# Optimization experiments

Hardware: AMD Instinct MI355X
Metric: run time of the kernel (lower is better)

The kernel has to match this reference:

```python
import jax, jax.numpy as jnp
import numpy as np

HIDDEN = 256
HEADS = 8
DK = HIDDEN // HEADS
BH = 16  # bias_h_size
N = 2048
B = 1


def setup_inputs() -> dict:
    key = jax.random.key(0)
    ks = jax.random.split(key, 20)
    s = 0.02
    inp = {
        "int_chain_label": jax.random.randint(ks[0], (N, N), 0, 2, dtype=jnp.int32),
        "dist_map": jax.random.uniform(ks[1], (N, N), dtype=jnp.float32),
        "contact_map": jax.random.uniform(ks[2], (N, N), dtype=jnp.float32),
        "q": jax.random.normal(ks[3], (B, N, HIDDEN), dtype=jnp.float32),
        "k": jax.random.normal(ks[4], (B, N, HIDDEN), dtype=jnp.float32),
        "v": jax.random.normal(ks[5], (B, N, HIDDEN), dtype=jnp.float32),
        # projections
        "Wq": jax.random.normal(ks[6], (HIDDEN, HIDDEN), dtype=jnp.float32) * s,
        "bq": jnp.zeros((HIDDEN,), jnp.float32),
        "Wk": jax.random.normal(ks[7], (HIDDEN, HIDDEN), dtype=jnp.float32) * s,
        "bk": jnp.zeros((HIDDEN,), jnp.float32),
        "Wv": jax.random.normal(ks[8], (HIDDEN, HIDDEN), dtype=jnp.float32) * s,
        "bv": jnp.zeros((HIDDEN,), jnp.float32),
        "Wo": jax.random.normal(ks[9], (HIDDEN, HIDDEN), dtype=jnp.float32) * s,
        "bo": jnp.zeros((HIDDEN,), jnp.float32),
        # distance bias MLP: Linear(2, BH) -> Linear(BH, 1)
        "Wd1": jax.random.normal(ks[10], (2, BH), dtype=jnp.float32) * 0.5,
        "bd1": jnp.zeros((BH,), jnp.float32),
        "Wd2": jax.random.normal(ks[11], (BH, 1), dtype=jnp.float32) * 0.5,
        "bd2": jnp.zeros((1,), jnp.float32),
        # contact bias MLP
        "Wc1": jax.random.normal(ks[12], (2, BH), dtype=jnp.float32) * 0.5,
        "bc1": jnp.zeros((BH,), jnp.float32),
        "Wc2": jax.random.normal(ks[13], (BH, 1), dtype=jnp.float32) * 0.5,
        "bc2": jnp.zeros((1,), jnp.float32),
    }
    return inp


def _pair_bias(mp, label_f, W1, b1, W2, b2):
    # stack(map, label) -> [N,N,2]; two linears (no nonlinearity in original) -> [N,N]
    x = jnp.stack((mp, label_f), axis=-1)
    h = x @ W1 + b1                      # [N,N,BH]
    return (h @ W2 + b2)[..., 0]          # [N,N]


def reference(int_chain_label, dist_map, contact_map, q, k, v,
              Wq, bq, Wk, bk, Wv, bv, Wo, bo,
              Wd1, bd1, Wd2, bd2, Wc1, bc1, Wc2, bc2):
    label_f = int_chain_label.astype(jnp.float32)
    bias = (_pair_bias(dist_map, label_f, Wd1, bd1, Wd2, bd2)
            + _pair_bias(contact_map, label_f, Wc1, bc1, Wc2, bc2))  # [N,N]
    bias = bias[None, None]  # [1,1,N,N] broadcast over batch, heads

    b, n, _ = q.shape
    scale = DK ** -0.5
    qh = (q @ Wq + bq).reshape(b, n, HEADS, DK).transpose(0, 2, 1, 3) * scale  # [B,H,N,D]
    kh = (k @ Wk + bk).reshape(b, n, HEADS, DK).transpose(0, 2, 1, 3)
    vh = (v @ Wv + bv).reshape(b, n, HEADS, DK).transpose(0, 2, 1, 3)

    scores = jnp.einsum('bhnd,bhmd->bhnm', qh, kh) + bias  # [B,H,N,N]
    attn = jax.nn.softmax(scores, axis=-1)
    out = jnp.einsum('bhnm,bhmd->bhnd', attn, vh)           # [B,H,N,D]
    out = out.transpose(0, 2, 1, 3).reshape(b, n, HEADS * DK)
    return out @ Wo + bo
```

## Files before the change

### kernel.cpp

```cpp
#include <hip/hip_runtime.h>
#include <hip/hip_bf16.h>

#define SN 2048
#define HD 256
#define NHEAD 8
#define DK 32
#define BH 16

typedef __bf16 bf16;
typedef __bf16 bf16x8 __attribute__((ext_vector_type(8)));
typedef __bf16 bf16x4 __attribute__((ext_vector_type(4)));
typedef float f32x4 __attribute__((ext_vector_type(4)));
typedef int i32x4 __attribute__((ext_vector_type(4)));
typedef unsigned uint4v __attribute__((ext_vector_type(4)));

__global__ void __launch_bounds__(256) prep_wt_kernel(
    const float* __restrict__ Wq, const float* __restrict__ Wk,
    const float* __restrict__ Wv, const float* __restrict__ Wo,
    bf16* __restrict__ wt)
{
    __shared__ bf16 tile[32][HD + 8];
    int mat = blockIdx.x >> 3, rc = blockIdx.x & 7;
    int t = threadIdx.x;
    const float* W = mat == 0 ? Wq : mat == 1 ? Wk : mat == 2 ? Wv : Wo;
    bf16* Wt = wt + mat * HD * HD;
    int r0 = rc * 32;
    #pragma unroll
    for (int i = 0; i < 32; i++) tile[i][t] = (bf16)W[(r0 + i) * HD + t];
    __syncthreads();
    #pragma unroll
    for (int i = 0; i < 32; i++) Wt[t * HD + r0 + i] = tile[i][t];
}

template<bool AF32, int MODE, bool OUTF32>
__device__ __forceinline__ void gemm_body(
    const void* __restrict__ Ap, const bf16* __restrict__ Wt,
    const float* __restrict__ bias, void* __restrict__ outp, int bid)
{
    int wave = threadIdx.x >> 6, lane = threadIdx.x & 63;
    int g = lane >> 4, qi = lane & 15;
    int mblk = bid & 31, nblk = bid >> 5;
    int m0 = mblk * 64 + wave * 16, n0 = nblk * 32;
    f32x4 acc0 = {0.f, 0.f, 0.f, 0.f}, acc1 = {0.f, 0.f, 0.f, 0.f};
    const bf16* W0 = Wt + (n0 + qi) * HD + 8 * g;
    const bf16* W1 = W0 + 16 * HD;

    auto loadA = [&](int ks) -> bf16x8 {
        if constexpr (AF32) {
            const float* Ar = (const float*)Ap + (m0 + qi) * HD + 8 * g + ks * 32;
            f32x4 lo = *(const f32x4*)Ar;
            f32x4 hi = *(const f32x4*)(Ar + 4);
            bf16x8 a;
            #pragma unroll
            for (int e = 0; e < 4; e++) { a[e] = (bf16)lo[e]; a[4 + e] = (bf16)hi[e]; }
            return a;
        } else {
            return *(const bf16x8*)((const bf16*)Ap + (m0 + qi) * HD + 8 * g + ks * 32);
        }
    };

    bf16x8 a_c  = loadA(0);
    bf16x8 b0_c = *(const bf16x8*)(W0);
    bf16x8 b1_c = *(const bf16x8*)(W1);
    #pragma unroll
    for (int ks = 0; ks < 8; ks++) {
        bf16x8 a_n, b0_n, b1_n;
        if (ks < 7) {
            a_n  = loadA(ks + 1);
            b0_n = *(const bf16x8*)(W0 + (ks + 1) * 32);
            b1_n = *(const bf16x8*)(W1 + (ks + 1) * 32);
        }
        acc0 = __builtin_amdgcn_mfma_f32_16x16x32_bf16(a_c, b0_c, acc0, 0, 0, 0);
        acc1 = __builtin_amdgcn_mfma_f32_16x16x32_bf16(a_c, b1_c, acc1, 0, 0, 0);
        if (ks < 7) { a_c = a_n; b0_c = b0_n; b1_c = b1_n; }
    }
    float bv0 = bias[n0 + qi], bv1 = bias[n0 + 16 + qi];
    if constexpr (MODE == 0) {
        if constexpr (OUTF32) {
            float* out = (float*)outp;
            #pragma unroll
            for (int r = 0; r < 4; r++) {
                int m = m0 + 4 * g + r;
                out[m * HD + n0 + qi]      = acc0[r] + bv0;
                out[m * HD + n0 + 16 + qi] = acc1[r] + bv1;
            }
        } else {
            bf16* out = (bf16*)outp;
            #pragma unroll
            for (int r = 0; r < 4; r++) {
                int m = m0 + 4 * g + r;
                out[m * HD + n0 + qi]      = (bf16)(acc0[r] + bv0);
                out[m * HD + n0 + 16 + qi] = (bf16)(acc1[r] + bv1);
            }
        }
    } else {
        bf16* out = (bf16*)outp;
        bf16x4 v0, v1;
        #pragma unroll
        for (int r = 0; r < 4; r++) { v0[r] = (bf16)(acc0[r] + bv0); v1[r] = (bf16)(acc1[r] + bv1); }
        *(bf16x4*)(out + (n0 + qi) * SN + m0 + 4 * g)      = v0;
        *(bf16x4*)(out + (n0 + 16 + qi) * SN + m0 + 4 * g) = v1;
    }
}

__global__ void __launch_bounds__(256) qkv_kernel(
    const float* __restrict__ q, const float* __restrict__ k, const float* __restrict__ v,
    const bf16* __restrict__ wt,
    const float* __restrict__ bq, const float* __restrict__ bk, const float* __restrict__ bv,
    bf16* __restrict__ qh, bf16* __restrict__ kh, bf16* __restrict__ vt)
{
    int w = blockIdx.y;
    if (w == 0)      gemm_body<true, 0, false>(q, wt,               bq, qh, blockIdx.x);
    else if (w == 1) gemm_body<true, 0, false>(k, wt + HD * HD,     bk, kh, blockIdx.x);
    else             gemm_body<true, 1, false>(v, wt + 2 * HD * HD, bv, vt, blockIdx.x);
}

__global__ void __launch_bounds__(256) oproj_kernel(
    const bf16* __restrict__ A, const bf16* __restrict__ wt3,
    const float* __restrict__ bo, float* __restrict__ out)
{
    gemm_body<false, 0, true>(A, wt3, bo, out, blockIdx.x);
}

template<int KCHT>
__global__ void __launch_bounds__(128) attn_kernel(
    const bf16* __restrict__ qh, const bf16* __restrict__ kh,
    const bf16* __restrict__ vt,
    const int* __restrict__ label, const float* __restrict__ dist,
    const float* __restrict__ contact,
    const float* __restrict__ Wd1, const float* __restrict__ bd1,
    const float* __restrict__ Wd2, const float* __restrict__ bd2,
    const float* __restrict__ Wc1, const float* __restrict__ bc1,
    const float* __restrict__ Wc2, const float* __restrict__ bc2,
    float* __restrict__ po, float* __restrict__ pm, float* __restrict__ pl)
{
    constexpr int KT = SN / KCHT / 64;
    int wave = threadIdx.x >> 6, lane = threadIdx.x & 63;
    int g = lane >> 4, qi = lane & 15;
    int h = blockIdx.x / (64 * KCHT);
    int rem = blockIdx.x % (64 * KCHT);
    int qb = rem / KCHT, c = rem % KCHT;
    int q0 = qb * 32 + wave * 16;
    int kbase = c * (KT * 64);

    float ad = 0.f, bld = 0.f, dd = bd2[0];
    #pragma unroll
    for (int j = 0; j < BH; j++) {
        float w2 = Wd2[j];
        ad  += Wd1[j] * w2;
        bld += Wd1[BH + j] * w2;
        dd  += bd1[j] * w2;
    }
    float ac = 0.f, blc = 0.f, dc = bc2[0];
    #pragma unroll
    for (int j = 0; j < BH; j++) {
        float w2 = Wc2[j];
        ac  += Wc1[j] * w2;
        blc += Wc1[BH + j] * w2;
        dc  += bc1[j] * w2;
    }
    float bl = bld + blc, dl = dd + dc;

    bf16x8 qf = *(const bf16x8*)(qh + (q0 + qi) * HD + h * DK + 8 * g);
    const bf16* kp  = kh + h * DK + 8 * g + kbase * HD;
    const bf16* v0p = vt + (h * DK + qi) * SN + 8 * g + kbase;
    const bf16* v1p = v0p + 16 * SN;
    const float* dp = dist    + (q0 + qi) * SN + 4 * g + kbase;
    const float* cp = contact + (q0 + qi) * SN + 4 * g + kbase;
    const int*   lp = label   + (q0 + qi) * SN + 4 * g + kbase;

    const float scale = 0.17677669529663687f;
    float m = -1e30f, lsum = 0.f;
    f32x4 o0 = {0.f, 0.f, 0.f, 0.f}, o1 = {0.f, 0.f, 0.f, 0.f};

    int src0 = ((lane >> 4) & 1) * 32 + (lane & 15);
    int src1 = src0 + 16;
    bool hi = lane >= 32;

    #pragma unroll
    for (int kt = 0; kt < KT; kt++) {
        int key0 = kt * 64;
        bf16x8 kf0 = *(const bf16x8*)(kp + (key0 +  0 + qi) * HD);
        bf16x8 kf1 = *(const bf16x8*)(kp + (key0 + 16 + qi) * HD);
        bf16x8 kf2 = *(const bf16x8*)(kp + (key0 + 32 + qi) * HD);
        bf16x8 kf3 = *(const bf16x8*)(kp + (key0 + 48 + qi) * HD);
        f32x4 dv0 = *(const f32x4*)(dp + key0 +  0), dv1 = *(const f32x4*)(dp + key0 + 16);
        f32x4 dv2 = *(const f32x4*)(dp + key0 + 32), dv3 = *(const f32x4*)(dp + key0 + 48);
        f32x4 cv0 = *(const f32x4*)(cp + key0 +  0), cv1 = *(const f32x4*)(cp + key0 + 16);
        f32x4 cv2 = *(const f32x4*)(cp + key0 + 32), cv3 = *(const f32x4*)(cp + key0 + 48);
        i32x4 lv0 = *(const i32x4*)(lp + key0 +  0), lv1 = *(const i32x4*)(lp + key0 + 16);
        i32x4 lv2 = *(const i32x4*)(lp + key0 + 32), lv3 = *(const i32x4*)(lp + key0 + 48);
        bf16x8 va00 = *(const bf16x8*)(v0p + key0);
        bf16x8 va01 = *(const bf16x8*)(v0p + key0 + 32);
        bf16x8 va10 = *(const bf16x8*)(v1p + key0);
        bf16x8 va11 = *(const bf16x8*)(v1p + key0 + 32);

        f32x4 zero = {0.f, 0.f, 0.f, 0.f};
        f32x4 s0 = __builtin_amdgcn_mfma_f32_16x16x32_bf16(kf0, qf, zero, 0, 0, 0);
        f32x4 s1 = __builtin_amdgcn_mfma_f32_16x16x32_bf16(kf1, qf, zero, 0, 0, 0);
        f32x4 s2 = __builtin_amdgcn_mfma_f32_16x16x32_bf16(kf2, qf, zero, 0, 0, 0);
        f32x4 s3 = __builtin_amdgcn_mfma_f32_16x16x32_bf16(kf3, qf, zero, 0, 0, 0);
        float x[16];
        #pragma unroll
        for (int r = 0; r < 4; r++) {
            float b0 = ad * dv0[r] + ac * cv0[r] + bl * (float)lv0[r] + dl;
            float b1 = ad * dv1[r] + ac * cv1[r] + bl * (float)lv1[r] + dl;
            float b2 = ad * dv2[r] + ac * cv2[r] + bl * (float)lv2[r] + dl;
            float b3 = ad * dv3[r] + ac * cv3[r] + bl * (float)lv3[r] + dl;
            x[r]      = s0[r] * scale + b0;
            x[4 + r]  = s1[r] * scale + b1;
            x[8 + r]  = s2[r] * scale + b2;
            x[12 + r] = s3[r] * scale + b3;
        }
        float t0 = fmaxf(x[0], x[1]),   t1 = fmaxf(x[2], x[3]);
        float t2 = fmaxf(x[4], x[5]),   t3 = fmaxf(x[6], x[7]);
        float t4 = fmaxf(x[8], x[9]),   t5 = fmaxf(x[10], x[11]);
        float t6 = fmaxf(x[12], x[13]), t7 = fmaxf(x[14], x[15]);
        float tm = fmaxf(fmaxf(fmaxf(t0, t1), fmaxf(t2, t3)),
                         fmaxf(fmaxf(t4, t5), fmaxf(t6, t7)));
        tm = fmaxf(tm, __shfl_xor(tm, 16));
        tm = fmaxf(tm, __shfl_xor(tm, 32));
        float mnew = fmaxf(m, tm);
        float f = __expf(m - mnew);
        float ps = 0.f;
        #pragma unroll
        for (int i = 0; i < 16; i++) { x[i] = __expf(x[i] - mnew); ps += x[i]; }
        ps += __shfl_xor(ps, 16);
        ps += __shfl_xor(ps, 32);
        lsum = lsum * f + ps;
        m = mnew;
        #pragma unroll
        for (int r = 0; r < 4; r++) { o0[r] *= f; o1[r] *= f; }

        auto PK = [](float a, float b) -> int {
            unsigned short ua = __builtin_bit_cast(unsigned short, (bf16)a);
            unsigned short ub = __builtin_bit_cast(unsigned short, (bf16)b);
            return (int)((unsigned)ua | ((unsigned)ub << 16));
        };
        int c0 = PK(x[0], x[1]),  c1 = PK(x[2], x[3]);
        int c2 = PK(x[4], x[5]),  c3 = PK(x[6], x[7]);
        int c4 = PK(x[8], x[9]),  c5 = PK(x[10], x[11]);
        int c6 = PK(x[12], x[13]), c7 = PK(x[14], x[15]);

        unsigned a00 = (unsigned)__shfl(c0, src0), a01 = (unsigned)__shfl(c2, src0);
        unsigned a10 = (unsigned)__shfl(c1, src0), a11 = (unsigned)__shfl(c3, src0);
        unsigned a20 = (unsigned)__shfl(c0, src1), a21 = (unsigned)__shfl(c2, src1);
        unsigned a30 = (unsigned)__shfl(c1, src1), a31 = (unsigned)__shfl(c3, src1);
        unsigned b00 = (unsigned)__shfl(c4, src0), b01 = (unsigned)__shfl(c6, src0);
        unsigned b10 = (unsigned)__shfl(c5, src0), b11 = (unsigned)__shfl(c7, src0);
        unsigned b20 = (unsigned)__shfl(c4, src1), b21 = (unsigned)__shfl(c6, src1);
        unsigned b30 = (unsigned)__shfl(c5, src1), b31 = (unsigned)__shfl(c7, src1);
        uint4v u0 = { hi ? a01 : a00, hi ? a11 : a10, hi ? a21 : a20, hi ? a31 : a30 };
        uint4v u1 = { hi ? b01 : b00, hi ? b11 : b10, hi ? b21 : b20, hi ? b31 : b30 };
        bf16x8 pb0 = __builtin_bit_cast(bf16x8, u0);
        bf16x8 pb1 = __builtin_bit_cast(bf16x8, u1);

        o0 = __builtin_amdgcn_mfma_f32_16x16x32_bf16(va00, pb0, o0, 0, 0, 0);
        o0 = __builtin_amdgcn_mfma_f32_16x16x32_bf16(va01, pb1, o0, 0, 0, 0);
        o1 = __builtin_amdgcn_mfma_f32_16x16x32_bf16(va10, pb0, o1, 0, 0, 0);
        o1 = __builtin_amdgcn_mfma_f32_16x16x32_bf16(va11, pb1, o1, 0, 0, 0);
    }
    int hq = h * SN + q0 + qi;
    *(f32x4*)(po + (hq * KCHT + c) * DK + 4 * g)      = o0;
    *(f32x4*)(po + (hq * KCHT + c) * DK + 16 + 4 * g) = o1;
    if (g == 0) { pm[hq * KCHT + c] = m; pl[hq * KCHT + c] = lsum; }
}

template<int KCHT>
__global__ void __launch_bounds__(256) combine_kernel(
    const float* __restrict__ po, const float* __restrict__ pm,
    const float* __restrict__ pl, bf16* __restrict__ aout)
{
    int idx = blockIdx.x * 256 + threadIdx.x;
    int d = idx & (DK - 1), hq = idx >> 5;
    int h = hq >> 11, qr = hq & (SN - 1);
    float mv[KCHT], lv[KCHT];
    #pragma unroll
    for (int c = 0; c < KCHT; c++) { mv[c] = pm[hq * KCHT + c]; lv[c] = pl[hq * KCHT + c]; }
    float M = mv[0];
    #pragma unroll
    for (int c = 1; c < KCHT; c++) M = fmaxf(M, mv[c]);
    float L = 0.f, o = 0.f;
    const float* p = po + hq * KCHT * DK + d;
    #pragma unroll
    for (int c = 0; c < KCHT; c++) {
        float w = __expf(mv[c] - M);
        L += w * lv[c];
        o += w * p[c * DK];
    }
    aout[qr * HD + h * DK + d] = (bf16)(o / L);
}

extern "C" void kernel_launch(void* const* d_in, const int* in_sizes, int n_in,
                              void* d_out, int out_size, void* d_ws, size_t ws_size,
                              hipStream_t stream)
{
    static const int expect[22] = {
        SN * SN, SN * SN, SN * SN,
        SN * HD, SN * HD, SN * HD,
        HD * HD, HD, HD * HD, HD,
        HD * HD, HD, HD * HD, HD,
        2 * BH, BH, BH, 1,
        2 * BH, BH, BH, 1
    };
    if (n_in != 22) return;
    for (int i = 0; i < 22; i++) if (in_sizes[i] != expect[i]) return;

    const int*   label   = (const int*)  d_in[0];
    const float* dist    = (const float*)d_in[1];
    const float* contact = (const float*)d_in[2];
    const float* q  = (const float*)d_in[3];
    const float* k  = (const float*)d_in[4];
    const float* v  = (const float*)d_in[5];
    const float* Wq = (const float*)d_in[6];  const float* bq = (const float*)d_in[7];
    const float* Wk = (const float*)d_in[8];  const float* bk = (const float*)d_in[9];
    const float* Wv = (const float*)d_in[10]; const float* bv = (const float*)d_in[11];
    const float* Wo = (const float*)d_in[12]; const float* bo = (const float*)d_in[13];
    const float* Wd1 = (const float*)d_in[14]; const float* bd1 = (const float*)d_in[15];
    const float* Wd2 = (const float*)d_in[16]; const float* bd2 = (const float*)d_in[17];
    const float* Wc1 = (const float*)d_in[18]; const float* bc1 = (const float*)d_in[19];
    const float* Wc2 = (const float*)d_in[20]; const float* bc2 = (const float*)d_in[21];

    char* ws = (char*)d_ws;
    bf16*  qh   = (bf16*)(ws);
    bf16*  kh   = (bf16*)(ws + (1u << 20));
    bf16*  vt   = (bf16*)(ws + (2u << 20));
    bf16*  aout = (bf16*)(ws + (3u << 20));
    bf16*  wt   = (bf16*)(ws + (4u << 20));
    float* po   = (float*)(ws + (5u << 20));

    prep_wt_kernel<<<dim3(32), 256, 0, stream>>>(Wq, Wk, Wv, Wo, wt);
    qkv_kernel<<<dim3(256, 3), 256, 0, stream>>>(q, k, v, wt, bq, bk, bv, qh, kh, vt);

    size_t need8 = (5u << 20) + (size_t)NHEAD * SN * 8 * DK * 4 + 2u * NHEAD * SN * 8 * 4;
    if (ws_size >= need8 + (1u << 20)) {
        float* pm = (float*)(ws + (5u << 20) + (size_t)NHEAD * SN * 8 * DK * 4);
        float* pl = pm + NHEAD * SN * 8;
        attn_kernel<8><<<dim3(NHEAD * 64 * 8), 128, 0, stream>>>(
            qh, kh, vt, label, dist, contact,
            Wd1, bd1, Wd2, bd2, Wc1, bc1, Wc2, bc2, po, pm, pl);
        combine_kernel<8><<<dim3(NHEAD * SN * DK / 256), 256, 0, stream>>>(po, pm, pl, aout);
    } else {
        float* pm = (float*)(ws + (13u << 20));
        float* pl = pm + NHEAD * SN * 4;
        attn_kernel<4><<<dim3(NHEAD * 64 * 4), 128, 0, stream>>>(
            qh, kh, vt, label, dist, contact,
            Wd1, bd1, Wd2, bd2, Wc1, bc1, Wc2, bc2, po, pm, pl);
        combine_kernel<4><<<dim3(NHEAD * SN * DK / 256), 256, 0, stream>>>(po, pm, pl, aout);
    }

    oproj_kernel<<<dim3(256), 256, 0, stream>>>(aout, wt + 3 * HD * HD, bo, (float*)d_out);
}
```

Baseline: 222.7 us.

## Precompute head-shared pair bias plane once instead of per-head

Adds a prep stage that collapses the dist, contact and label maps into a single fp32 bias plane, written to the workspace before attention. The attention kernel then reads one float stream per key instead of three and skips the per-element bias arithmetic, which was previously repeated for each of the 8 heads. This costs an extra read of three N×N maps and a write of one N×N plane up front, and needs more workspace. A fallback path keeps the old inline computation for small workspaces.

```diff
diff --git a/kernel.cpp b/kernel.cpp
--- a/kernel.cpp
+++ b/kernel.cpp
@@ -14,22 +14,62 @@
 typedef int i32x4 __attribute__((ext_vector_type(4)));
 typedef unsigned uint4v __attribute__((ext_vector_type(4)));
 
-__global__ void __launch_bounds__(256) prep_wt_kernel(
+__global__ void __launch_bounds__(256) prep_kernel(
     const float* __restrict__ Wq, const float* __restrict__ Wk,
     const float* __restrict__ Wv, const float* __restrict__ Wo,
-    bf16* __restrict__ wt)
-{
-    __shared__ bf16 tile[32][HD + 8];
-    int mat = blockIdx.x >> 3, rc = blockIdx.x & 7;
+    const int* __restrict__ label, const float* __restrict__ dist,
+    const float* __restrict__ contact,
+    const float* __restrict__ Wd1, const float* __restrict__ bd1,
+    const float* __restrict__ Wd2, const float* __restrict__ bd2,
+    const float* __restrict__ Wc1, const float* __restrict__ bc1,
+    const float* __restrict__ Wc2, const float* __restrict__ bc2,
+    bf16* __restrict__ wt, float* __restrict__ plane)
+{
+    int bid = blockIdx.x;
     int t = threadIdx.x;
-    const float* W = mat == 0 ? Wq : mat == 1 ? Wk : mat == 2 ? Wv : Wo;
-    bf16* Wt = wt + mat * HD * HD;
-    int r0 = rc * 32;
-    #pragma unroll
-    for (int i = 0; i < 32; i++) tile[i][t] = (bf16)W[(r0 + i) * HD + t];
-    __syncthreads();
-    #pragma unroll
-    for (int i = 0; i < 32; i++) Wt[t * HD + r0 + i] = tile[i][t];
+    if (bid < 32) {
+        __shared__ bf16 tile[32][HD + 8];
+        int mat = bid >> 3, rc = bid & 7;
+        const float* W = mat == 0 ? Wq : mat == 1 ? Wk : mat == 2 ? Wv : Wo;
+        bf16* Wt = wt + mat * HD * HD;
+        int r0 = rc * 32;
+        #pragma unroll
+        for (int i = 0; i < 32; i++) tile[i][t] = (bf16)W[(r0 + i) * HD + t];
+        __syncthreads();
+        #pragma unroll
+        for (int i = 0; i < 32; i++) Wt[t * HD + r0 + i] = tile[i][t];
+        return;
+    }
+    float ad = 0.f, bld = 0.f, dd = bd2[0];
+    #pragma unroll
+    for (int j = 0; j < BH; j++) {
+        float w2 = Wd2[j];
+        ad  += Wd1[j] * w2;
+        bld += Wd1[BH + j] * w2;
+        dd  += bd1[j] * w2;
+    }
+    float ac = 0.f, blc = 0.f, dc = bc2[0];
+    #pragma unroll
+    for (int j = 0; j < BH; j++) {
+        float w2 = Wc2[j];
+        ac  += Wc1[j] * w2;
+        blc += Wc1[BH + j] * w2;
+        dc  += bc1[j] * w2;
+    }
+    float bl = bld + blc, dl = dd + dc;
+
+    int base = (bid - 32) * 2048 + t * 8;
+    f32x4 d0 = *(const f32x4*)(dist + base),    d1 = *(const f32x4*)(dist + base + 4);
+    f32x4 c0 = *(const f32x4*)(contact + base), c1 = *(const f32x4*)(contact + base + 4);
+    i32x4 l0 = *(const i32x4*)(label + base),   l1 = *(const i32x4*)(label + base + 4);
+    f32x4 o0, o1;
+    #pragma unroll
+    for (int e = 0; e < 4; e++) {
+        o0[e] = ad * d0[e] + ac * c0[e] + bl * (float)l0[e] + dl;
+        o1[e] = ad * d1[e] + ac * c1[e] + bl * (float)l1[e] + dl;
+    }
+    *(f32x4*)(plane + base)     = o0;
+    *(f32x4*)(plane + base + 4) = o1;
 }
 
 template<bool AF32, int MODE, bool OUTF32>
@@ -122,10 +162,10 @@
     gemm_body<false, 0, true>(A, wt3, bo, out, blockIdx.x);
 }
 
-template<int KCHT>
+template<int KCHT, bool PLANE>
 __global__ void __launch_bounds__(128) attn_kernel(
     const bf16* __restrict__ qh, const bf16* __restrict__ kh,
-    const bf16* __restrict__ vt,
+    const bf16* __restrict__ vt, const float* __restrict__ plane,
     const int* __restrict__ label, const float* __restrict__ dist,
     const float* __restrict__ contact,
     const float* __restrict__ Wd1, const float* __restrict__ bd1,
@@ -143,28 +183,32 @@
     int q0 = qb * 32 + wave * 16;
     int kbase = c * (KT * 64);
 
-    float ad = 0.f, bld = 0.f, dd = bd2[0];
-    #pragma unroll
-    for (int j = 0; j < BH; j++) {
-        float w2 = Wd2[j];
-        ad  += Wd1[j] * w2;
-        bld += Wd1[BH + j] * w2;
-        dd  += bd1[j] * w2;
-    }
-    float ac = 0.f, blc = 0.f, dc = bc2[0];
-    #pragma unroll
-    for (int j = 0; j < BH; j++) {
-        float w2 = Wc2[j];
-        ac  += Wc1[j] * w2;
-        blc += Wc1[BH + j] * w2;
-        dc  += bc1[j] * w2;
-    }
-    float bl = bld + blc, dl = dd + dc;
+    float ad = 0.f, bl = 0.f, acoef = 0.f, dl = 0.f;
+    if constexpr (!PLANE) {
+        float bld = 0.f, dd = bd2[0];
+        #pragma unroll
+        for (int j = 0; j < BH; j++) {
+            float w2 = Wd2[j];
+            ad  += Wd1[j] * w2;
+            bld += Wd1[BH + j] * w2;
+            dd  += bd1[j] * w2;
+        }
+        float blc = 0.f, dc = bc2[0];
+        #pragma unroll
+        for (int j = 0; j < BH; j++) {
+            float w2 = Wc2[j];
+            acoef += Wc1[j] * w2;
+            blc   += Wc1[BH + j] * w2;
+            dc    += bc1[j] * w2;
+        }
+        bl = bld + blc; dl = dd + dc;
+    }
 
     bf16x8 qf = *(const bf16x8*)(qh + (q0 + qi) * HD + h * DK + 8 * g);
     const bf16* kp  = kh + h * DK + 8 * g + kbase * HD;
     const bf16* v0p = vt + (h * DK + qi) * SN + 8 * g + kbase;
     const bf16* v1p = v0p + 16 * SN;
+    const float* bp = plane   + (q0 + qi) * SN + 4 * g + kbase;
     const float* dp = dist    + (q0 + qi) * SN + 4 * g + kbase;
     const float* cp = contact + (q0 + qi) * SN + 4 * g + kbase;
     const int*   lp = label   + (q0 + qi) * SN + 4 * g + kbase;
@@ -184,12 +228,21 @@
         bf16x8 kf1 = *(const bf16x8*)(kp + (key0 + 16 + qi) * HD);
         bf16x8 kf2 = *(const bf16x8*)(kp + (key0 + 32 + qi) * HD);
         bf16x8 kf3 = *(const bf16x8*)(kp + (key0 + 48 + qi) * HD);
-        f32x4 dv0 = *(const f32x4*)(dp + key0 +  0), dv1 = *(const f32x4*)(dp + key0 + 16);
-        f32x4 dv2 = *(const f32x4*)(dp + key0 + 32), dv3 = *(const f32x4*)(dp + key0 + 48);
-        f32x4 cv0 = *(const f32x4*)(cp + key0 +  0), cv1 = *(const f32x4*)(cp + key0 + 16);
-        f32x4 cv2 = *(const f32x4*)(cp + key0 + 32), cv3 = *(const f32x4*)(cp + key0 + 48);
-        i32x4 lv0 = *(const i32x4*)(lp + key0 +  0), lv1 = *(const i32x4*)(lp + key0 + 16);
-        i32x4 lv2 = *(const i32x4*)(lp + key0 + 32), lv3 = *(const i32x4*)(lp + key0 + 48);
+        f32x4 bv[4];
+        if constexpr (PLANE) {
+            #pragma unroll
+            for (int s = 0; s < 4; s++) bv[s] = *(const f32x4*)(bp + key0 + 16 * s);
+        } else {
+            #pragma unroll
+            for (int s = 0; s < 4; s++) {
+                f32x4 dv = *(const f32x4*)(dp + key0 + 16 * s);
+                f32x4 cv = *(const f32x4*)(cp + key0 + 16 * s);
+                i32x4 lv = *(const i32x4*)(lp + key0 + 16 * s);
+                #pragma unroll
+                for (int r = 0; r < 4; r++)
+                    bv[s][r] = ad * dv[r] + acoef * cv[r] + bl * (float)lv[r] + dl;
+            }
+        }
         bf16x8 va00 = *(const bf16x8*)(v0p + key0);
         bf16x8 va01 = *(const bf16x8*)(v0p + key0 + 32);
         bf16x8 va10 = *(const bf16x8*)(v1p + key0);
@@ -203,14 +256,10 @@
         float x[16];
         #pragma unroll
         for (int r = 0; r < 4; r++) {
-            float b0 = ad * dv0[r] + ac * cv0[r] + bl * (float)lv0[r] + dl;
-            float b1 = ad * dv1[r] + ac * cv1[r] + bl * (float)lv1[r] + dl;
-            float b2 = ad * dv2[r] + ac * cv2[r] + bl * (float)lv2[r] + dl;
-            float b3 = ad * dv3[r] + ac * cv3[r] + bl * (float)lv3[r] + dl;
-            x[r]      = s0[r] * scale + b0;
-            x[4 + r]  = s1[r] * scale + b1;
-            x[8 + r]  = s2[r] * scale + b2;
-            x[12 + r] = s3[r] * scale + b3;
+            x[r]      = s0[r] * scale + bv[0][r];
+            x[4 + r]  = s1[r] * scale + bv[1][r];
+            x[8 + r]  = s2[r] * scale + bv[2][r];
+            x[12 + r] = s3[r] * scale + bv[3][r];
         }
         float t0 = fmaxf(x[0], x[1]),   t1 = fmaxf(x[2], x[3]);
         float t2 = fmaxf(x[4], x[5]),   t3 = fmaxf(x[6], x[7]);
@@ -237,9 +286,9 @@
             unsigned short ub = __builtin_bit_cast(unsigned short, (bf16)b);
             return (int)((unsigned)ua | ((unsigned)ub << 16));
         };
-        int c0 = PK(x[0], x[1]),  c1 = PK(x[2], x[3]);
-        int c2 = PK(x[4], x[5]),  c3 = PK(x[6], x[7]);
-        int c4 = PK(x[8], x[9]),  c5 = PK(x[10], x[11]);
+        int c0 = PK(x[0], x[1]),   c1 = PK(x[2], x[3]);
+        int c2 = PK(x[4], x[5]),   c3 = PK(x[6], x[7]);
+        int c4 = PK(x[8], x[9]),   c5 = PK(x[10], x[11]);
         int c6 = PK(x[12], x[13]), c7 = PK(x[14], x[15]);
 
         unsigned a00 = (unsigned)__shfl(c0, src0), a01 = (unsigned)__shfl(c2, src0);
@@ -321,32 +370,45 @@
     const float* Wc1 = (const float*)d_in[18]; const float* bc1 = (const float*)d_in[19];
     const float* Wc2 = (const float*)d_in[20]; const float* bc2 = (const float*)d_in[21];
 
+    const size_t MB = 1u << 20;
     char* ws = (char*)d_ws;
-    bf16*  qh   = (bf16*)(ws);
-    bf16*  kh   = (bf16*)(ws + (1u << 20));
-    bf16*  vt   = (bf16*)(ws + (2u << 20));
-    bf16*  aout = (bf16*)(ws + (3u << 20));
-    bf16*  wt   = (bf16*)(ws + (4u << 20));
-    float* po   = (float*)(ws + (5u << 20));
-
-    prep_wt_kernel<<<dim3(32), 256, 0, stream>>>(Wq, Wk, Wv, Wo, wt);
+    bf16*  qh    = (bf16*)(ws);
+    bf16*  kh    = (bf16*)(ws + 1 * MB);
+    bf16*  vt    = (bf16*)(ws + 2 * MB);
+    bf16*  aout  = (bf16*)(ws + 3 * MB);
+    bf16*  wt    = (bf16*)(ws + 4 * MB);
+    float* plane = (float*)(ws + 5 * MB);
+
+    prep_kernel<<<dim3(32 + SN * SN / 2048), 256, 0, stream>>>(
+        Wq, Wk, Wv, Wo, label, dist, contact,
+        Wd1, bd1, Wd2, bd2, Wc1, bc1, Wc2, bc2, wt, plane);
+
     qkv_kernel<<<dim3(256, 3), 256, 0, stream>>>(q, k, v, wt, bq, bk, bv, qh, kh, vt);
 
-    size_t need8 = (5u << 20) + (size_t)NHEAD * SN * 8 * DK * 4 + 2u * NHEAD * SN * 8 * 4;
-    if (ws_size >= need8 + (1u << 20)) {
-        float* pm = (float*)(ws + (5u << 20) + (size_t)NHEAD * SN * 8 * DK * 4);
+    if (ws_size >= 38 * MB) {
+        float* po = (float*)(ws + 21 * MB);
+        float* pm = (float*)(ws + 37 * MB);
         float* pl = pm + NHEAD * SN * 8;
-        attn_kernel<8><<<dim3(NHEAD * 64 * 8), 128, 0, stream>>>(
-            qh, kh, vt, label, dist, contact,
+        attn_kernel<8, true><<<dim3(NHEAD * 64 * 8), 128, 0, stream>>>(
+            qh, kh, vt, plane, label, dist, contact,
             Wd1, bd1, Wd2, bd2, Wc1, bc1, Wc2, bc2, po, pm, pl);
         combine_kernel<8><<<dim3(NHEAD * SN * DK / 256), 256, 0, stream>>>(po, pm, pl, aout);
-    } else {
-        float* pm = (float*)(ws + (13u << 20));
+    } else if (ws_size >= 30 * MB) {
+        float* po = (float*)(ws + 21 * MB);
+        float* pm = (float*)(ws + 29 * MB);
         float* pl = pm + NHEAD * SN * 4;
-        attn_kernel<4><<<dim3(NHEAD * 64 * 4), 128, 0, stream>>>(
-            qh, kh, vt, label, dist, contact,
+        attn_kernel<4, true><<<dim3(NHEAD * 64 * 4), 128, 0, stream>>>(
+            qh, kh, vt, plane, label, dist, contact,
             Wd1, bd1, Wd2, bd2, Wc1, bc1, Wc2, bc2, po, pm, pl);
         combine_kernel<4><<<dim3(NHEAD * SN * DK / 256), 256, 0, stream>>>(po, pm, pl, aout);
+    } else {
+        float* po = (float*)(ws + 5 * MB);
+        float* pm = (float*)(ws + 21 * MB);
+        float* pl = pm + NHEAD * SN * 8;
+        attn_kernel<8, false><<<dim3(NHEAD * 64 * 8), 128, 0, stream>>>(
+            qh, kh, vt, plane, label, dist, contact,
+            Wd1, bd1, Wd2, bd2, Wc1, bc1, Wc2, bc2, po, pm, pl);
+        combine_kernel<8><<<dim3(NHEAD * SN * DK / 256), 256, 0, stream>>>(po, pm, pl, aout);
     }
 
     oproj_kernel<<<dim3(256), 256, 0, stream>>>(aout, wt + 3 * HD * HD, bo, (float*)d_out);
```

After: 199.7 us. -10.3%, faster.
